# Performance work log

Measured on AMD Instinct MI355X. Metric: run time of the kernel, lower is better.

Reference implementation:

```python
import jax, jax.numpy as jnp
import numpy as np
import math

DIM = 2048
N_HEADS = 16
HEAD_DIM = DIM // N_HEADS  # 128
SEQ = 2048
EPS = 1e-5
NEG = -1e9


def get_slopes(n):
    # n is a power of 2 here (16)
    start = 2.0 ** (-2.0 ** (-(math.log2(n) - 3)))
    return [start * start ** i for i in range(n)]


def setup_inputs() -> dict:
    key = jax.random.key(0)
    ks = jax.random.split(key, 6)
    x = jax.random.normal(ks[0], (1, SEQ, DIM), dtype=jnp.float32)
    # causal additive mask (large negative above diagonal)
    causal = jnp.tril(jnp.ones((SEQ, SEQ), dtype=bool))
    mask = jnp.where(causal, 0.0, NEG).astype(jnp.float32)[None, None]
    scale_w = 0.02
    wq = jax.random.normal(ks[1], (DIM, DIM), dtype=jnp.float32) * scale_w  # [in, out]
    wk = jax.random.normal(ks[2], (DIM, DIM), dtype=jnp.float32) * scale_w
    wv = jax.random.normal(ks[3], (DIM, DIM), dtype=jnp.float32) * scale_w
    wo = jax.random.normal(ks[4], (DIM, DIM), dtype=jnp.float32) * scale_w
    # AttentionPrior params: shape_init=1, scale_init='slope' (stored as log), loc_init=0
    shape = jnp.ones((1, N_HEADS, 1, 1), dtype=jnp.float32)
    scale = jnp.log(jnp.asarray(get_slopes(N_HEADS), dtype=jnp.float32)).reshape(1, N_HEADS, 1, 1)
    loc = jnp.zeros((1, N_HEADS, 1, 1), dtype=jnp.float32)
    return {"x": x, "mask": mask, "wq": wq, "wk": wk, "wv": wv, "wo": wo,
            "shape": shape, "scale": scale, "loc": loc, "start_pos": 0}


def _prior_bias(shape, scale, loc, seqlen, start_pos):
    q_pos = jnp.arange(seqlen, dtype=jnp.float32) + start_pos
    k_pos = jnp.arange(seqlen + start_pos, dtype=jnp.float32)
    dist = (k_pos[None, :] - q_pos[:, None])[None, None]  # [1,1,S,K]
    loc_t = jnp.exp(loc) - jnp.exp(-loc)
    z = (dist - loc_t) * jnp.exp(scale)  # [1,H,S,K]
    return -(jnp.abs(z) + EPS) ** shape


def reference(x, mask, wq, wk, wv, wo, shape, scale, loc, start_pos):
    bsz, seqlen, _ = x.shape
    q = (x @ wq).reshape(bsz, seqlen, N_HEADS, HEAD_DIM)
    k = (x @ wk).reshape(bsz, seqlen, N_HEADS, HEAD_DIM)
    v = (x @ wv).reshape(bsz, seqlen, N_HEADS, HEAD_DIM)
    # start_pos=0 prefill: cache slice == current keys/values
    scores = jnp.einsum('bqhd,bkhd->bhqk', q, k) / math.sqrt(HEAD_DIM)
    scores = scores + _prior_bias(shape, scale, loc, seqlen, start_pos)
    scores = scores + mask
    probs = jax.nn.softmax(scores.astype(jnp.float32), axis=-1).astype(q.dtype)
    out = jnp.einsum('bhqk,bkhd->bqhd', probs, v).reshape(bsz, seqlen, DIM)
    return out @ wo
```

## Files before the change

kernel.cpp:

```cpp
#include <hip/hip_runtime.h>
#include <hip/hip_bf16.h>
#include <stdint.h>


typedef unsigned short u16;
typedef unsigned int u32;

using bf16x8  = __attribute__((ext_vector_type(8))) __bf16;
using f32x4   = __attribute__((ext_vector_type(4))) float;
using f32x16  = __attribute__((ext_vector_type(16))) float;

__device__ __forceinline__ u16 f2bf(float f) {
  union { float f; u32 u; } v; v.f = f;
  u32 r = (v.u + 0x7FFFu + ((v.u >> 16) & 1u)) >> 16;
  return (u16)r;
}

__device__ __forceinline__ u16 f2bfn(float f) {
  union { __bf16 b; u16 u; } c; c.b = (__bf16)f; return c.u;
}

__device__ __forceinline__ float bf2f(u16 h) {
  union { u32 u; float f; } v; v.u = ((u32)h) << 16; return v.f;
}

__device__ __forceinline__ void gload16(const void* g, void* l) {
  __builtin_amdgcn_global_load_lds((const __attribute__((address_space(1))) void*)g,
                                   (__attribute__((address_space(3))) void*)l, 16, 0, 0);
}

__device__ __forceinline__ int cumch128(int qt) {
  if (qt < 4)  return qt;
  if (qt < 8)  return 4 + 2 * (qt - 4);
  if (qt < 12) return 12 + 3 * (qt - 8);
  return 24 + 4 * (qt - 12);
}

__global__ __launch_bounds__(256) void prep(const float* __restrict__ x, const float* __restrict__ wq,
                                            const float* __restrict__ wk, const float* __restrict__ wv,
                                            const float* __restrict__ wo,
                                            u16* __restrict__ xb, u16* __restrict__ wqkt,
                                            u16* __restrict__ wvt, u16* __restrict__ wot) {
  __shared__ float tile[32][33];
  const int z = blockIdx.z;
  const int t = threadIdx.x;
  if (z == 4) {
    int i = ((blockIdx.y * 64 + blockIdx.x) * 256 + t);
    float4 v = ((const float4*)x)[i];
    ushort4 o;
    o.x = f2bf(v.x); o.y = f2bf(v.y); o.z = f2bf(v.z); o.w = f2bf(v.w);
    ((ushort4*)xb)[i] = o;
    return;
  }
  const float* src = (z == 0) ? wq : (z == 1) ? wk : (z == 2) ? wv : wo;
  u16* dst = (z == 0) ? wqkt : (z == 1) ? (wqkt + 2048 * 2048) : (z == 2) ? wvt : wot;
  const int c0 = blockIdx.x * 32, r0 = blockIdx.y * 32;
  const int ci = t & 31, rj = t >> 5;
#pragma unroll
  for (int j = 0; j < 4; ++j)
    tile[rj + j * 8][ci] = src[(size_t)(r0 + rj + j * 8) * 2048 + c0 + ci];
  __syncthreads();
#pragma unroll
  for (int j = 0; j < 4; ++j) {
    int rr = rj + j * 8;
    dst[(size_t)(c0 + rr) * 2048 + r0 + ci] = f2bf(tile[ci][rr]);
  }
}

__global__ __launch_bounds__(256) void gemm_qkv(const u16* __restrict__ xb, const u16* __restrict__ wqkt,
                                                const u16* __restrict__ wvt,
                                                u16* __restrict__ qkc, u16* __restrict__ vtc) {
  __shared__ u16 lds[16384];
  int bid = blockIdx.x;
  const u16 *A, *Bt;
  u16* C;
  int N, bn, bm, scl_cols;
  if (bid < 512) { A = xb;  Bt = wqkt; C = qkc; N = 4096; bn = bid & 31; bm = bid >> 5; scl_cols = 2048; }
  else { bid -= 512; A = wvt; Bt = xb; C = vtc; N = 2048; bn = bid & 15; bm = bid >> 4; scl_cols = 0; }
  const int K = 2048;

  const int t = threadIdx.x;
  const int w = t >> 6, l = t & 63;
  const int wm = w >> 1, wn = w & 1;
  const int lrow = l & 15, lgrp = l >> 4;

  f32x4 acc[4][4] = {};

  for (int k0 = 0; k0 < K; k0 += 64) {
    if (k0) __syncthreads();
#pragma unroll
    for (int p = 0; p < 4; ++p) {
      int i = (p * 4 + w) * 64 + l;
      int r = i >> 3, u = i & 7;
      const u16* src = A + (size_t)(bm * 128 + r) * K + k0 + ((u ^ (r & 7)) << 3);
      gload16(src, (char*)lds + (p * 4 + w) * 1024);
    }
#pragma unroll
    for (int p = 0; p < 4; ++p) {
      int i = (p * 4 + w) * 64 + l;
      int r = i >> 3, u = i & 7;
      const u16* src = Bt + (size_t)(bn * 128 + r) * K + k0 + ((u ^ (r & 7)) << 3);
      gload16(src, (char*)lds + 16384 + (p * 4 + w) * 1024);
    }
    __syncthreads();

#pragma unroll
    for (int kc = 0; kc < 2; ++kc) {
      bf16x8 af[4], bfr[4];
#pragma unroll
      for (int mt = 0; mt < 4; ++mt) {
        int rho = wm * 64 + mt * 16 + lrow;
        int un = (kc * 4 + lgrp) ^ (rho & 7);
        af[mt] = *(const bf16x8*)((const char*)lds + rho * 128 + un * 16);
      }
#pragma unroll
      for (int nt = 0; nt < 4; ++nt) {
        int rho = wn * 64 + nt * 16 + lrow;
        int un = (kc * 4 + lgrp) ^ (rho & 7);
        bfr[nt] = *(const bf16x8*)((const char*)lds + 16384 + rho * 128 + un * 16);
      }
#pragma unroll
      for (int mt = 0; mt < 4; ++mt)
#pragma unroll
        for (int nt = 0; nt < 4; ++nt)
          acc[mt][nt] = __builtin_amdgcn_mfma_f32_16x16x32_bf16(af[mt], bfr[nt], acc[mt][nt], 0, 0, 0);
    }
  }

  const int row0 = bm * 128 + wm * 64;
  const int col0 = bn * 128 + wn * 64;
#pragma unroll
  for (int mt = 0; mt < 4; ++mt)
#pragma unroll
    for (int nt = 0; nt < 4; ++nt) {
      int col = col0 + nt * 16 + lrow;
      float s = (col < scl_cols) ? 0.08838834764831843f : 1.0f;
#pragma unroll
      for (int r = 0; r < 4; ++r) {
        int row = row0 + mt * 16 + lgrp * 4 + r;
        C[(size_t)row * N + col] = f2bf(acc[mt][nt][r] * s);
      }
    }
}

__global__ __launch_bounds__(256) void gemm_outk(const u16* __restrict__ A, const u16* __restrict__ Bt,
                                                 u16* __restrict__ P0, u16* __restrict__ P1) {
  __shared__ u16 lds[16384];
  const int b = blockIdx.x;
  const int z = b >> 8;
  const int bn = b & 15, bm = (b >> 4) & 15;
  u16* C = z ? P1 : P0;
  const int K = 2048;
  const int kbeg = z * 1024, kend = kbeg + 1024;

  const int t = threadIdx.x;
  const int w = t >> 6, l = t & 63;
  const int wm = w >> 1, wn = w & 1;
  const int lrow = l & 15, lgrp = l >> 4;

  f32x4 acc[4][4] = {};

  for (int k0 = kbeg; k0 < kend; k0 += 64) {
    if (k0 != kbeg) __syncthreads();
#pragma unroll
    for (int p = 0; p < 4; ++p) {
      int i = (p * 4 + w) * 64 + l;
      int r = i >> 3, u = i & 7;
      const u16* src = A + (size_t)(bm * 128 + r) * K + k0 + ((u ^ (r & 7)) << 3);
      gload16(src, (char*)lds + (p * 4 + w) * 1024);
    }
#pragma unroll
    for (int p = 0; p < 4; ++p) {
      int i = (p * 4 + w) * 64 + l;
      int r = i >> 3, u = i & 7;
      const u16* src = Bt + (size_t)(bn * 128 + r) * K + k0 + ((u ^ (r & 7)) << 3);
      gload16(src, (char*)lds + 16384 + (p * 4 + w) * 1024);
    }
    __syncthreads();

#pragma unroll
    for (int kc = 0; kc < 2; ++kc) {
      bf16x8 af[4], bfr[4];
#pragma unroll
      for (int mt = 0; mt < 4; ++mt) {
        int rho = wm * 64 + mt * 16 + lrow;
        int un = (kc * 4 + lgrp) ^ (rho & 7);
        af[mt] = *(const bf16x8*)((const char*)lds + rho * 128 + un * 16);
      }
#pragma unroll
      for (int nt = 0; nt < 4; ++nt) {
        int rho = wn * 64 + nt * 16 + lrow;
        int un = (kc * 4 + lgrp) ^ (rho & 7);
        bfr[nt] = *(const bf16x8*)((const char*)lds + 16384 + rho * 128 + un * 16);
      }
#pragma unroll
      for (int mt = 0; mt < 4; ++mt)
#pragma unroll
        for (int nt = 0; nt < 4; ++nt)
          acc[mt][nt] = __builtin_amdgcn_mfma_f32_16x16x32_bf16(af[mt], bfr[nt], acc[mt][nt], 0, 0, 0);
    }
  }

  const int row0 = bm * 128 + wm * 64;
  const int col0 = bn * 128 + wn * 64;
#pragma unroll
  for (int mt = 0; mt < 4; ++mt)
#pragma unroll
    for (int nt = 0; nt < 4; ++nt) {
      int col = col0 + nt * 16 + lrow;
#pragma unroll
      for (int r = 0; r < 4; ++r) {
        int row = row0 + mt * 16 + lgrp * 4 + r;
        C[(size_t)row * 2048 + col] = f2bf(acc[mt][nt][r]);
      }
    }
}

__global__ __launch_bounds__(256) void combine_out(const u16* __restrict__ P0, const u16* __restrict__ P1,
                                                   float* __restrict__ out) {
  const int i = blockIdx.x * 256 + threadIdx.x;
  uint4 a = ((const uint4*)P0)[i];
  uint4 b = ((const uint4*)P1)[i];
  float4 o0, o1;
  o0.x = bf2f(a.x & 0xFFFF) + bf2f(b.x & 0xFFFF); o0.y = bf2f(a.x >> 16) + bf2f(b.x >> 16);
  o0.z = bf2f(a.y & 0xFFFF) + bf2f(b.y & 0xFFFF); o0.w = bf2f(a.y >> 16) + bf2f(b.y >> 16);
  o1.x = bf2f(a.z & 0xFFFF) + bf2f(b.z & 0xFFFF); o1.y = bf2f(a.z >> 16) + bf2f(b.z >> 16);
  o1.z = bf2f(a.w & 0xFFFF) + bf2f(b.w & 0xFFFF); o1.w = bf2f(a.w >> 16) + bf2f(b.w >> 16);
  ((float4*)out)[i * 2]     = o0;
  ((float4*)out)[i * 2 + 1] = o1;
}

__global__ __launch_bounds__(256) void attn_part(const u16* __restrict__ QK, const u16* __restrict__ Vt,
                                                 u16* __restrict__ Opart, float* __restrict__ Lpart,
                                                 const float* __restrict__ g_shape,
                                                 const float* __restrict__ g_scale,
                                                 const float* __restrict__ g_loc,
                                                 const int* __restrict__ g_sp) {
  __shared__ u16 k_lds[2][4096];
  __shared__ u16 v_lds[2][4096];
  __shared__ u16 p_lds[4][1280];

  const int raw = blockIdx.x;
  const int bid = (raw & 7) * 80 + (raw >> 3);
  const int h = bid / 40;
  const int rem = bid - h * 40;
  int qt, ch;
  if (rem < 4)       { qt = rem;                 ch = 0; }
  else if (rem < 12) { int r2 = rem - 4;  qt = 4  + (r2 >> 1); ch = r2 & 1; }
  else if (rem < 24) { int r3 = rem - 12; qt = 8  + r3 / 3;    ch = r3 - 3 * (r3 / 3); }
  else               { int r4 = rem - 24; qt = 12 + (r4 >> 2); ch = r4 & 3; }
  const int pid = bid;

  const int t = threadIdx.x, w = t >> 6, l = t & 63;
  const int lc = l & 31, lh = l >> 5;

  const float sh = g_shape[h];
  const float es = __expf(g_scale[h]);
  const float lcv = g_loc[h];
  const float loc_t = __expf(lcv) - __expf(-lcv);
  const int sp = g_sp[0];
  const bool shape1 = (sh == 1.0f);

  const int qwave = qt * 128 + w * 32;

  bf16x8 qf[8];
  {
    const u16* qp = QK + (size_t)(qwave + lc) * 4096 + h * 128 + lh * 8;
#pragma unroll
    for (int ks = 0; ks < 8; ++ks) qf[ks] = *(const bf16x8*)(qp + ks * 16);
  }

  f32x16 o[4] = {};
  float lr[16];
#pragma unroll
  for (int r = 0; r < 16; ++r) lr[r] = 0.0f;

  const int kstart = ch * 16;
  const int kend = min(kstart + 16, 4 * qt + 4);

#define STAGE_TILE(buf, kt_) do {                                                        \
    const int kv0s = (kt_) * 32;                                                         \
    _Pragma("unroll")                                                                    \
    for (int p = 0; p < 2; ++p) {                                                        \
      int i = p * 256 + t;                                                               \
      int r = i >> 4, u = i & 15;                                                        \
      const u16* src = QK + (size_t)(kv0s + r) * 4096 + 2048 + h * 128 + ((u ^ (r & 7)) << 3); \
      gload16(src, (char*)k_lds[buf] + (p * 256 + w * 64) * 16);                         \
    }                                                                                    \
    _Pragma("unroll")                                                                    \
    for (int p = 0; p < 2; ++p) {                                                        \
      int i = p * 256 + t;                                                               \
      int r = i >> 2, u = i & 3;                                                         \
      const u16* src = Vt + (size_t)(h * 128 + r) * 2048 + kv0s + ((u ^ ((r >> 2) & 3)) << 3); \
      gload16(src, (char*)v_lds[buf] + (p * 256 + w * 64) * 16);                         \
    }                                                                                    \
  } while (0)

  STAGE_TILE(0, kstart);
  __syncthreads();

  for (int kt = kstart; kt < kend; ++kt) {
    const int cur = (kt - kstart) & 1;
    if (kt + 1 < kend) STAGE_TILE(cur ^ 1, kt + 1);
    const int kv0 = kt * 32;

    f32x16 s;
#pragma unroll
    for (int r = 0; r < 16; ++r) s[r] = -11.0f;
#pragma unroll
    for (int ks = 0; ks < 8; ++ks) {
      int un = (ks * 2 + lh) ^ (lc & 7);
      bf16x8 bk = *(const bf16x8*)((const char*)k_lds[cur] + lc * 256 + un * 16);
      s = __builtin_amdgcn_mfma_f32_32x32x16_bf16(qf[ks], bk, s, 0, 0, 0);
    }

    const float fdb = (float)(kv0 + lc - (qwave + 4 * lh) - sp);
    const float fb = fdb - loc_t;
    const bool need_mask = (kv0 + 31 > qwave + sp);
    if (shape1 && !need_mask) {
#pragma unroll
      for (int r = 0; r < 16; ++r) {
        const float rowoff = (float)((r & 3) + 8 * (r >> 2));
        float u = fb - rowoff;
        float p = __expf(fmaf(-es, fabsf(u), s[r]));
        lr[r] += p;
        p_lds[w][((r & 3) + 8 * (r >> 2) + 4 * lh) * 40 + lc] = f2bfn(p);
      }
    } else if (shape1) {
#pragma unroll
      for (int r = 0; r < 16; ++r) {
        const float rowoff = (float)((r & 3) + 8 * (r >> 2));
        float u = fb - rowoff;
        float p = __expf(fmaf(-es, fabsf(u), s[r]));
        p = (fdb > rowoff) ? 0.0f : p;
        lr[r] += p;
        p_lds[w][((r & 3) + 8 * (r >> 2) + 4 * lh) * 40 + lc] = f2bfn(p);
      }
    } else {
#pragma unroll
      for (int r = 0; r < 16; ++r) {
        const float rowoff = (float)((r & 3) + 8 * (r >> 2));
        float u = fb - rowoff;
        float az = fmaf(es, fabsf(u), 1e-5f);
        float p = __expf(s[r] - __powf(az, sh));
        p = (fdb > rowoff) ? 0.0f : p;
        lr[r] += p;
        p_lds[w][((r & 3) + 8 * (r >> 2) + 4 * lh) * 40 + lc] = f2bfn(p);
      }
    }

    bf16x8 pa0 = *(const bf16x8*)((const char*)p_lds[w] + lc * 80 + lh * 16);
    bf16x8 pa1 = *(const bf16x8*)((const char*)p_lds[w] + lc * 80 + 32 + lh * 16);
#pragma unroll
    for (int dc = 0; dc < 4; ++dc) {
      int row0 = dc * 32 + lc;
      int un0 = (lh) ^ ((row0 >> 2) & 3);
      int un1 = (2 + lh) ^ ((row0 >> 2) & 3);
      bf16x8 bv0 = *(const bf16x8*)((const char*)v_lds[cur] + row0 * 64 + un0 * 16);
      bf16x8 bv1 = *(const bf16x8*)((const char*)v_lds[cur] + row0 * 64 + un1 * 16);
      o[dc] = __builtin_amdgcn_mfma_f32_32x32x16_bf16(pa0, bv0, o[dc], 0, 0, 0);
      o[dc] = __builtin_amdgcn_mfma_f32_32x32x16_bf16(pa1, bv1, o[dc], 0, 0, 0);
    }

    __syncthreads();
  }
#undef STAGE_TILE

#pragma unroll
  for (int r = 0; r < 16; ++r) {
#pragma unroll
    for (int msk = 1; msk <= 16; msk <<= 1) lr[r] += __shfl_xor(lr[r], msk);
  }

  u16* ob = Opart + (size_t)pid * 16384;
#pragma unroll
  for (int dc = 0; dc < 4; ++dc) {
#pragma unroll
    for (int r = 0; r < 16; ++r) {
      int row = w * 32 + (r & 3) + 8 * (r >> 2) + 4 * lh;
      ob[(size_t)row * 128 + dc * 32 + lc] = f2bfn(o[dc][r]);
    }
  }
  if (lc == 0) {
#pragma unroll
    for (int r = 0; r < 16; ++r) {
      int row = w * 32 + (r & 3) + 8 * (r >> 2) + 4 * lh;
      Lpart[(size_t)pid * 128 + row] = lr[r];
    }
  }
}

__global__ __launch_bounds__(256) void attn_merge(const u16* __restrict__ Opart,
                                                  const float* __restrict__ Lpart,
                                                  u16* __restrict__ AO) {
  const int bid = blockIdx.x;
  const int qt = bid & 15, h = bid >> 4;
  const int nch = (qt >> 2) + 1;
  const int base = h * 40 + cumch128(qt);
  const int t = threadIdx.x;
  const int row = t >> 1;
  const int dseg = (t & 1) << 6;

  float acc[64] = {};
  float lstar = 0.0f;
#pragma unroll
  for (int i = 0; i < 4; ++i) {
    if (i < nch) {
      lstar += Lpart[(size_t)(base + i) * 128 + row];
      const ushort4* op = (const ushort4*)(Opart + (size_t)(base + i) * 16384 + row * 128 + dseg);
#pragma unroll
      for (int j = 0; j < 16; ++j) {
        ushort4 v = op[j];
        acc[j * 4 + 0] += bf2f(v.x); acc[j * 4 + 1] += bf2f(v.y);
        acc[j * 4 + 2] += bf2f(v.z); acc[j * 4 + 3] += bf2f(v.w);
      }
    }
  }
  const float inv = 1.0f / lstar;
  const int q_abs = qt * 128 + row;
  u16* dst = AO + (size_t)q_abs * 2048 + h * 128 + dseg;
#pragma unroll
  for (int j = 0; j < 16; ++j) {
    ushort4 ov;
    ov.x = f2bf(acc[j * 4 + 0] * inv); ov.y = f2bf(acc[j * 4 + 1] * inv);
    ov.z = f2bf(acc[j * 4 + 2] * inv); ov.w = f2bf(acc[j * 4 + 3] * inv);
    *(ushort4*)(dst + j * 4) = ov;
  }
}

extern "C" void kernel_launch(void* const* d_in, const int* in_sizes, int n_in,
                              void* d_out, int out_size, void* d_ws, size_t ws_size,
                              hipStream_t stream) {
  const float* x   = (const float*)d_in[0];
  const float* wq  = (const float*)d_in[2];
  const float* wk  = (const float*)d_in[3];
  const float* wv  = (const float*)d_in[4];
  const float* wo  = (const float*)d_in[5];
  const float* shp = (const float*)d_in[6];
  const float* scl = (const float*)d_in[7];
  const float* loc = (const float*)d_in[8];
  const int*   sp  = (const int*)d_in[9];

  char* ws = (char*)d_ws;
  u16*   xb    = (u16*)(ws);
  u16*   wqkt  = (u16*)(ws + (size_t)( 8u << 20));
  u16*   wvt   = (u16*)(ws + (size_t)(24u << 20));
  u16*   opart = (u16*)(ws);
  u16*   wot   = (u16*)(ws + (size_t)(40u << 20));
  u16*   qk    = (u16*)(ws + (size_t)(48u << 20));
  u16*   pc0   = (u16*)(ws + (size_t)(48u << 20));
  u16*   pc1   = (u16*)(ws + (size_t)(56u << 20));
  u16*   vt    = (u16*)(ws + (size_t)(64u << 20));
  u16*   ao    = (u16*)(ws + (size_t)(72u << 20));
  float* lpart = (float*)(ws + (size_t)(80u << 20));

  hipLaunchKernelGGL(prep, dim3(64, 64, 5), dim3(256), 0, stream,
                     x, wq, wk, wv, wo, xb, wqkt, wvt, wot);
  hipLaunchKernelGGL(gemm_qkv, dim3(768), dim3(256), 0, stream, xb, wqkt, wvt, qk, vt);
  hipLaunchKernelGGL(attn_part, dim3(640), dim3(256), 0, stream,
                     qk, vt, opart, lpart, shp, scl, loc, sp);
  hipLaunchKernelGGL(attn_merge, dim3(256), dim3(256), 0, stream, opart, lpart, ao);
  hipLaunchKernelGGL(gemm_outk, dim3(512), dim3(256), 0, stream, ao, wot, pc0, pc1);
  hipLaunchKernelGGL(combine_out, dim3(2048), dim3(256), 0, stream, pc0, pc1, (float*)d_out);
}
```

Before: 171.0 us.

## Replace split-K output GEMM with 128x64 tiles; use 16x16 MFMA in attention

The output projection drops the split-K scheme (two bf16 partial buffers plus a combine kernel). It becomes a single GEMM over 128x64 tiles across a 32x16 grid that writes fp32 directly. This removes one launch and the partial-sum traffic, and avoids rounding the partials to bf16. Separately, the attention kernel switches from 32x32x16 MFMA to 16x16x32 MFMA with the matching fragment layouts, row-offset maths and LDS indexing. That changes register pressure and instruction mix, and may or may not help throughput.

```diff
diff --git a/kernel.cpp b/kernel.cpp
--- a/kernel.cpp
+++ b/kernel.cpp
@@ -6,9 +6,8 @@
 typedef unsigned short u16;
 typedef unsigned int u32;
 
-using bf16x8  = __attribute__((ext_vector_type(8))) __bf16;
-using f32x4   = __attribute__((ext_vector_type(4))) float;
-using f32x16  = __attribute__((ext_vector_type(16))) float;
+using bf16x8 = __attribute__((ext_vector_type(8))) __bf16;
+using f32x4  = __attribute__((ext_vector_type(4))) float;
 
 __device__ __forceinline__ u16 f2bf(float f) {
   union { float f; u32 u; } v; v.f = f;
@@ -143,44 +142,40 @@
     }
 }
 
-__global__ __launch_bounds__(256) void gemm_outk(const u16* __restrict__ A, const u16* __restrict__ Bt,
-                                                 u16* __restrict__ P0, u16* __restrict__ P1) {
-  __shared__ u16 lds[16384];
-  const int b = blockIdx.x;
-  const int z = b >> 8;
-  const int bn = b & 15, bm = (b >> 4) & 15;
-  u16* C = z ? P1 : P0;
+__global__ __launch_bounds__(256) void gemm_out(const u16* __restrict__ A, const u16* __restrict__ Bt,
+                                                float* __restrict__ out) {
+  __shared__ u16 lds[12288];
+  const int bn = blockIdx.x, bm = blockIdx.y;
   const int K = 2048;
-  const int kbeg = z * 1024, kend = kbeg + 1024;
 
   const int t = threadIdx.x;
   const int w = t >> 6, l = t & 63;
   const int wm = w >> 1, wn = w & 1;
   const int lrow = l & 15, lgrp = l >> 4;
 
-  f32x4 acc[4][4] = {};
-
-  for (int k0 = kbeg; k0 < kend; k0 += 64) {
-    if (k0 != kbeg) __syncthreads();
+  f32x4 acc[4][2] = {};
+
+  for (int k0 = 0; k0 < K; k0 += 64) {
+    if (k0) __syncthreads();
 #pragma unroll
     for (int p = 0; p < 4; ++p) {
-      int i = (p * 4 + w) * 64 + l;
+      int i = p * 256 + t;
       int r = i >> 3, u = i & 7;
       const u16* src = A + (size_t)(bm * 128 + r) * K + k0 + ((u ^ (r & 7)) << 3);
-      gload16(src, (char*)lds + (p * 4 + w) * 1024);
-    }
-#pragma unroll
-    for (int p = 0; p < 4; ++p) {
-      int i = (p * 4 + w) * 64 + l;
+      gload16(src, (char*)lds + i * 16);
+    }
+#pragma unroll
+    for (int p = 0; p < 2; ++p) {
+      int i = p * 256 + t;
       int r = i >> 3, u = i & 7;
-      const u16* src = Bt + (size_t)(bn * 128 + r) * K + k0 + ((u ^ (r & 7)) << 3);
-      gload16(src, (char*)lds + 16384 + (p * 4 + w) * 1024);
+      const u16* src = Bt + (size_t)(bn * 64 + r) * K + k0 + ((u ^ (r & 7)) << 3);
+      gload16(src, (char*)lds + 16384 + i * 16);
     }
     __syncthreads();
 
 #pragma unroll
     for (int kc = 0; kc < 2; ++kc) {
-      bf16x8 af[4], bfr[4];
+      bf16x8 af[4], bfr[2];
 #pragma unroll
       for (int mt = 0; mt < 4; ++mt) {
         int rho = wm * 64 + mt * 16 + lrow;
@@ -188,46 +183,32 @@
         af[mt] = *(const bf16x8*)((const char*)lds + rho * 128 + un * 16);
       }
 #pragma unroll
-      for (int nt = 0; nt < 4; ++nt) {
-        int rho = wn * 64 + nt * 16 + lrow;
+      for (int nt = 0; nt < 2; ++nt) {
+        int rho = wn * 32 + nt * 16 + lrow;
         int un = (kc * 4 + lgrp) ^ (rho & 7);
         bfr[nt] = *(const bf16x8*)((const char*)lds + 16384 + rho * 128 + un * 16);
       }
 #pragma unroll
       for (int mt = 0; mt < 4; ++mt)
 #pragma unroll
-        for (int nt = 0; nt < 4; ++nt)
+        for (int nt = 0; nt < 2; ++nt)
           acc[mt][nt] = __builtin_amdgcn_mfma_f32_16x16x32_bf16(af[mt], bfr[nt], acc[mt][nt], 0, 0, 0);
     }
   }
 
   const int row0 = bm * 128 + wm * 64;
-  const int col0 = bn * 128 + wn * 64;
+  const int col0 = bn * 64 + wn * 32;
 #pragma unroll
   for (int mt = 0; mt < 4; ++mt)
 #pragma unroll
-    for (int nt = 0; nt < 4; ++nt) {
+    for (int nt = 0; nt < 2; ++nt) {
       int col = col0 + nt * 16 + lrow;
 #pragma unroll
       for (int r = 0; r < 4; ++r) {
         int row = row0 + mt * 16 + lgrp * 4 + r;
-        C[(size_t)row * 2048 + col] = f2bf(acc[mt][nt][r]);
-      }
-    }
-}
-
-__global__ __launch_bounds__(256) void combine_out(const u16* __restrict__ P0, const u16* __restrict__ P1,
-                                                   float* __restrict__ out) {
-  const int i = blockIdx.x * 256 + threadIdx.x;
-  uint4 a = ((const uint4*)P0)[i];
-  uint4 b = ((const uint4*)P1)[i];
-  float4 o0, o1;
-  o0.x = bf2f(a.x & 0xFFFF) + bf2f(b.x & 0xFFFF); o0.y = bf2f(a.x >> 16) + bf2f(b.x >> 16);
-  o0.z = bf2f(a.y & 0xFFFF) + bf2f(b.y & 0xFFFF); o0.w = bf2f(a.y >> 16) + bf2f(b.y >> 16);
-  o1.x = bf2f(a.z & 0xFFFF) + bf2f(b.z & 0xFFFF); o1.y = bf2f(a.z >> 16) + bf2f(b.z >> 16);
-  o1.z = bf2f(a.w & 0xFFFF) + bf2f(b.w & 0xFFFF); o1.w = bf2f(a.w >> 16) + bf2f(b.w >> 16);
-  ((float4*)out)[i * 2]     = o0;
-  ((float4*)out)[i * 2 + 1] = o1;
+        out[(size_t)row * 2048 + col] = acc[mt][nt][r];
+      }
+    }
 }
 
 __global__ __launch_bounds__(256) void attn_part(const u16* __restrict__ QK, const u16* __restrict__ Vt,
@@ -252,7 +233,7 @@
   const int pid = bid;
 
   const int t = threadIdx.x, w = t >> 6, l = t & 63;
-  const int lc = l & 31, lh = l >> 5;
+  const int lrow = l & 15, lgrp = l >> 4;
 
   const float sh = g_shape[h];
   const float es = __expf(g_scale[h]);
@@ -263,17 +244,16 @@
 
   const int qwave = qt * 128 + w * 32;
 
-  bf16x8 qf[8];
-  {
-    const u16* qp = QK + (size_t)(qwave + lc) * 4096 + h * 128 + lh * 8;
-#pragma unroll
-    for (int ks = 0; ks < 8; ++ks) qf[ks] = *(const bf16x8*)(qp + ks * 16);
-  }
-
-  f32x16 o[4] = {};
-  float lr[16];
-#pragma unroll
-  for (int r = 0; r < 16; ++r) lr[r] = 0.0f;
+  bf16x8 qf[2][4];
+#pragma unroll
+  for (int mt = 0; mt < 2; ++mt) {
+    const u16* qp = QK + (size_t)(qwave + mt * 16 + lrow) * 4096 + h * 128 + lgrp * 8;
+#pragma unroll
+    for (int kc = 0; kc < 4; ++kc) qf[mt][kc] = *(const bf16x8*)(qp + kc * 32);
+  }
+
+  f32x4 o[2][8] = {};
+  float lr[2][4] = {};
 
   const int kstart = ch * 16;
   const int kend = min(kstart + 16, 4 * qt + 4);
@@ -285,14 +265,14 @@
       int i = p * 256 + t;                                                               \
       int r = i >> 4, u = i & 15;                                                        \
       const u16* src = QK + (size_t)(kv0s + r) * 4096 + 2048 + h * 128 + ((u ^ (r & 7)) << 3); \
-      gload16(src, (char*)k_lds[buf] + (p * 256 + w * 64) * 16);                         \
+      gload16(src, (char*)k_lds[buf] + i * 16);                                          \
     }                                                                                    \
     _Pragma("unroll")                                                                    \
     for (int p = 0; p < 2; ++p) {                                                        \
       int i = p * 256 + t;                                                               \
       int r = i >> 2, u = i & 3;                                                         \
       const u16* src = Vt + (size_t)(h * 128 + r) * 2048 + kv0s + ((u ^ ((r >> 2) & 3)) << 3); \
-      gload16(src, (char*)v_lds[buf] + (p * 256 + w * 64) * 16);                         \
+      gload16(src, (char*)v_lds[buf] + i * 16);                                          \
     }                                                                                    \
   } while (0)
 
@@ -304,62 +284,82 @@
     if (kt + 1 < kend) STAGE_TILE(cur ^ 1, kt + 1);
     const int kv0 = kt * 32;
 
-    f32x16 s;
-#pragma unroll
-    for (int r = 0; r < 16; ++r) s[r] = -11.0f;
-#pragma unroll
-    for (int ks = 0; ks < 8; ++ks) {
-      int un = (ks * 2 + lh) ^ (lc & 7);
-      bf16x8 bk = *(const bf16x8*)((const char*)k_lds[cur] + lc * 256 + un * 16);
-      s = __builtin_amdgcn_mfma_f32_32x32x16_bf16(qf[ks], bk, s, 0, 0, 0);
-    }
-
-    const float fdb = (float)(kv0 + lc - (qwave + 4 * lh) - sp);
-    const float fb = fdb - loc_t;
+    f32x4 s4[2][2];
+#pragma unroll
+    for (int mt = 0; mt < 2; ++mt)
+#pragma unroll
+      for (int nc = 0; nc < 2; ++nc) s4[mt][nc] = f32x4{-11.0f, -11.0f, -11.0f, -11.0f};
+#pragma unroll
+    for (int kc = 0; kc < 4; ++kc) {
+#pragma unroll
+      for (int nc = 0; nc < 2; ++nc) {
+        int rho = nc * 16 + lrow;
+        int un = (kc * 4 + lgrp) ^ (rho & 7);
+        bf16x8 bk = *(const bf16x8*)((const char*)k_lds[cur] + rho * 256 + un * 16);
+        s4[0][nc] = __builtin_amdgcn_mfma_f32_16x16x32_bf16(qf[0][kc], bk, s4[0][nc], 0, 0, 0);
+        s4[1][nc] = __builtin_amdgcn_mfma_f32_16x16x32_bf16(qf[1][kc], bk, s4[1][nc], 0, 0, 0);
+      }
+    }
+
     const bool need_mask = (kv0 + 31 > qwave + sp);
     if (shape1 && !need_mask) {
 #pragma unroll
-      for (int r = 0; r < 16; ++r) {
-        const float rowoff = (float)((r & 3) + 8 * (r >> 2));
-        float u = fb - rowoff;
-        float p = __expf(fmaf(-es, fabsf(u), s[r]));
-        lr[r] += p;
-        p_lds[w][((r & 3) + 8 * (r >> 2) + 4 * lh) * 40 + lc] = f2bfn(p);
-      }
+      for (int mt = 0; mt < 2; ++mt)
+#pragma unroll
+        for (int r = 0; r < 4; ++r) {
+          const float fb = (float)(kv0 + lrow - (qwave + mt * 16 + lgrp * 4 + r) - sp) - loc_t;
+#pragma unroll
+          for (int nc = 0; nc < 2; ++nc) {
+            float u = fb + (float)(nc * 16);
+            float p = __expf(fmaf(-es, fabsf(u), s4[mt][nc][r]));
+            lr[mt][r] += p;
+            p_lds[w][(mt * 16 + lgrp * 4 + r) * 40 + nc * 16 + lrow] = f2bfn(p);
+          }
+        }
     } else if (shape1) {
 #pragma unroll
-      for (int r = 0; r < 16; ++r) {
-        const float rowoff = (float)((r & 3) + 8 * (r >> 2));
-        float u = fb - rowoff;
-        float p = __expf(fmaf(-es, fabsf(u), s[r]));
-        p = (fdb > rowoff) ? 0.0f : p;
-        lr[r] += p;
-        p_lds[w][((r & 3) + 8 * (r >> 2) + 4 * lh) * 40 + lc] = f2bfn(p);
-      }
+      for (int mt = 0; mt < 2; ++mt)
+#pragma unroll
+        for (int r = 0; r < 4; ++r) {
+          const float fb = (float)(kv0 + lrow - (qwave + mt * 16 + lgrp * 4 + r) - sp) - loc_t;
+#pragma unroll
+          for (int nc = 0; nc < 2; ++nc) {
+            float u = fb + (float)(nc * 16);
+            float p = __expf(fmaf(-es, fabsf(u), s4[mt][nc][r]));
+            p = (u + loc_t > 0.0f) ? 0.0f : p;
+            lr[mt][r] += p;
+            p_lds[w][(mt * 16 + lgrp * 4 + r) * 40 + nc * 16 + lrow] = f2bfn(p);
+          }
+        }
     } else {
 #pragma unroll
-      for (int r = 0; r < 16; ++r) {
-        const float rowoff = (float)((r & 3) + 8 * (r >> 2));
-        float u = fb - rowoff;
-        float az = fmaf(es, fabsf(u), 1e-5f);
-        float p = __expf(s[r] - __powf(az, sh));
-        p = (fdb > rowoff) ? 0.0f : p;
-        lr[r] += p;
-        p_lds[w][((r & 3) + 8 * (r >> 2) + 4 * lh) * 40 + lc] = f2bfn(p);
-      }
-    }
-
-    bf16x8 pa0 = *(const bf16x8*)((const char*)p_lds[w] + lc * 80 + lh * 16);
-    bf16x8 pa1 = *(const bf16x8*)((const char*)p_lds[w] + lc * 80 + 32 + lh * 16);
-#pragma unroll
-    for (int dc = 0; dc < 4; ++dc) {
-      int row0 = dc * 32 + lc;
-      int un0 = (lh) ^ ((row0 >> 2) & 3);
-      int un1 = (2 + lh) ^ ((row0 >> 2) & 3);
-      bf16x8 bv0 = *(const bf16x8*)((const char*)v_lds[cur] + row0 * 64 + un0 * 16);
-      bf16x8 bv1 = *(const bf16x8*)((const char*)v_lds[cur] + row0 * 64 + un1 * 16);
-      o[dc] = __builtin_amdgcn_mfma_f32_32x32x16_bf16(pa0, bv0, o[dc], 0, 0, 0);
-      o[dc] = __builtin_amdgcn_mfma_f32_32x32x16_bf16(pa1, bv1, o[dc], 0, 0, 0);
+      for (int mt = 0; mt < 2; ++mt)
+#pragma unroll
+        for (int r = 0; r < 4; ++r) {
+          const float fb = (float)(kv0 + lrow - (qwave + mt * 16 + lgrp * 4 + r) - sp) - loc_t;
+#pragma unroll
+          for (int nc = 0; nc < 2; ++nc) {
+            float u = fb + (float)(nc * 16);
+            float az = fmaf(es, fabsf(u), 1e-5f);
+            float p = __expf(s4[mt][nc][r] - __powf(az, sh));
+            p = (u + loc_t > 0.0f) ? 0.0f : p;
+            lr[mt][r] += p;
+            p_lds[w][(mt * 16 + lgrp * 4 + r) * 40 + nc * 16 + lrow] = f2bfn(p);
+          }
+        }
+    }
+
+    {
+      bf16x8 pa0 = *(const bf16x8*)((const char*)p_lds[w] + lrow * 80 + lgrp * 16);
+      bf16x8 pa1 = *(const bf16x8*)((const char*)p_lds[w] + (16 + lrow) * 80 + lgrp * 16);
+#pragma unroll
+      for (int dc = 0; dc < 8; ++dc) {
+        int rho = dc * 16 + lrow;
+        int un = lgrp ^ ((rho >> 2) & 3);
+        bf16x8 bv = *(const bf16x8*)((const char*)v_lds[cur] + rho * 64 + un * 16);
+        o[0][dc] = __builtin_amdgcn_mfma_f32_16x16x32_bf16(pa0, bv, o[0][dc], 0, 0, 0);
+        o[1][dc] = __builtin_amdgcn_mfma_f32_16x16x32_bf16(pa1, bv, o[1][dc], 0, 0, 0);
+      }
     }
 
     __syncthreads();
@@ -367,26 +367,30 @@
 #undef STAGE_TILE
 
 #pragma unroll
-  for (int r = 0; r < 16; ++r) {
-#pragma unroll
-    for (int msk = 1; msk <= 16; msk <<= 1) lr[r] += __shfl_xor(lr[r], msk);
-  }
+  for (int mt = 0; mt < 2; ++mt)
+#pragma unroll
+    for (int r = 0; r < 4; ++r)
+#pragma unroll
+      for (int msk = 1; msk <= 8; msk <<= 1) lr[mt][r] += __shfl_xor(lr[mt][r], msk);
 
   u16* ob = Opart + (size_t)pid * 16384;
 #pragma unroll
-  for (int dc = 0; dc < 4; ++dc) {
-#pragma unroll
-    for (int r = 0; r < 16; ++r) {
-      int row = w * 32 + (r & 3) + 8 * (r >> 2) + 4 * lh;
-      ob[(size_t)row * 128 + dc * 32 + lc] = f2bfn(o[dc][r]);
-    }
-  }
-  if (lc == 0) {
-#pragma unroll
-    for (int r = 0; r < 16; ++r) {
-      int row = w * 32 + (r & 3) + 8 * (r >> 2) + 4 * lh;
-      Lpart[(size_t)pid * 128 + row] = lr[r];
-    }
+  for (int mt = 0; mt < 2; ++mt)
+#pragma unroll
+    for (int dc = 0; dc < 8; ++dc)
+#pragma unroll
+      for (int r = 0; r < 4; ++r) {
+        int row = w * 32 + mt * 16 + lgrp * 4 + r;
+        ob[(size_t)row * 128 + dc * 16 + lrow] = f2bfn(o[mt][dc][r]);
+      }
+  if (lrow == 0) {
+#pragma unroll
+    for (int mt = 0; mt < 2; ++mt)
+#pragma unroll
+      for (int r = 0; r < 4; ++r) {
+        int row = w * 32 + mt * 16 + lgrp * 4 + r;
+        Lpart[(size_t)pid * 128 + row] = lr[mt][r];
+      }
   }
 }
 
@@ -448,8 +452,6 @@
   u16*   opart = (u16*)(ws);
   u16*   wot   = (u16*)(ws + (size_t)(40u << 20));
   u16*   qk    = (u16*)(ws + (size_t)(48u << 20));
-  u16*   pc0   = (u16*)(ws + (size_t)(48u << 20));
-  u16*   pc1   = (u16*)(ws + (size_t)(56u << 20));
   u16*   vt    = (u16*)(ws + (size_t)(64u << 20));
   u16*   ao    = (u16*)(ws + (size_t)(72u << 20));
   float* lpart = (float*)(ws + (size_t)(80u << 20));
@@ -460,6 +462,5 @@
   hipLaunchKernelGGL(attn_part, dim3(640), dim3(256), 0, stream,
                      qk, vt, opart, lpart, shp, scl, loc, sp);
   hipLaunchKernelGGL(attn_merge, dim3(256), dim3(256), 0, stream, opart, lpart, ao);
-  hipLaunchKernelGGL(gemm_outk, dim3(512), dim3(256), 0, stream, ao, wot, pc0, pc1);
-  hipLaunchKernelGGL(combine_out, dim3(2048), dim3(256), 0, stream, pc0, pc1, (float*)d_out);
-}
+  hipLaunchKernelGGL(gemm_out, dim3(32, 16), dim3(256), 0, stream, ao, wot, (float*)d_out);
+}
```

After: 167.8 us. No clear change (-1.9%).
